# Optimization experiments

Measured on AMD Instinct MI355X. Metric: run time of the kernel, lower is better.

Reference implementation:

```python
import jax, jax.numpy as jnp
import numpy as np

IN_CH = 256
NUM_ANCHORS = 9
NUM_CLASSES = 91
PRIOR_P = 0.01


def conv3x3(x, w, b):
    # x: [N,C,H,W], w: [O,I,3,3], b: [O]
    y = jax.lax.conv_general_dilated(
        x, w, window_strides=(1, 1), padding='SAME',
        dimension_numbers=('NCHW', 'OIHW', 'NCHW'))
    return y + b[None, :, None, None]


def run_head(x, conv_w, conv_b, out_w, out_b, k):
    for i in range(4):
        x = jax.nn.relu(conv3x3(x, conv_w[i], conv_b[i]))
    y = conv3x3(x, out_w, out_b)
    n, _, h, w = y.shape
    # [N, A*k, H, W] -> [N, A, k, H, W] -> [N, H, W, A, k] -> [N, H*W*A, k]
    y = y.reshape(n, -1, k, h, w).transpose(0, 3, 4, 1, 2).reshape(n, -1, k)
    return y


def setup_inputs() -> dict:
    key = jax.random.key(0)
    ks = jax.random.split(key, 16)
    sizes = [128, 64, 32, 16, 8]
    inp = {}
    for i, s in enumerate(sizes):
        inp[f'feat{i}'] = jax.random.normal(ks[i], (2, IN_CH, s, s), dtype=jnp.float32)
    std = 0.01
    inp['cls_conv_w'] = std * jax.random.normal(ks[5], (4, IN_CH, IN_CH, 3, 3), dtype=jnp.float32)
    inp['cls_conv_b'] = jnp.zeros((4, IN_CH), dtype=jnp.float32)
    inp['cls_out_w'] = std * jax.random.normal(ks[6], (NUM_ANCHORS * NUM_CLASSES, IN_CH, 3, 3), dtype=jnp.float32)
    bias_init = -np.log((1.0 - PRIOR_P) / PRIOR_P)
    inp['cls_out_b'] = jnp.full((NUM_ANCHORS * NUM_CLASSES,), bias_init, dtype=jnp.float32)
    inp['reg_conv_w'] = std * jax.random.normal(ks[7], (4, IN_CH, IN_CH, 3, 3), dtype=jnp.float32)
    inp['reg_conv_b'] = jnp.zeros((4, IN_CH), dtype=jnp.float32)
    inp['reg_out_w'] = std * jax.random.normal(ks[8], (NUM_ANCHORS * 4, IN_CH, 3, 3), dtype=jnp.float32)
    inp['reg_out_b'] = jnp.zeros((NUM_ANCHORS * 4,), dtype=jnp.float32)
    return inp


def reference(feat0, feat1, feat2, feat3, feat4,
              cls_conv_w, cls_conv_b, cls_out_w, cls_out_b,
              reg_conv_w, reg_conv_b, reg_out_w, reg_out_b):
    feats = [feat0, feat1, feat2, feat3, feat4]
    cls_logits = jnp.concatenate(
        [run_head(f, cls_conv_w, cls_conv_b, cls_out_w, cls_out_b, NUM_CLASSES) for f in feats],
        axis=1)  # [N, sum(HWA), num_classes]
    bbox_regression = jnp.concatenate(
        [run_head(f, reg_conv_w, reg_conv_b, reg_out_w, reg_out_b, 4) for f in feats],
        axis=1)  # [N, sum(HWA), 4]
    return (cls_logits, bbox_regression)
```

## Files before the change

kernel.cpp:

```cpp
#include <hip/hip_runtime.h>
#include <hip/hip_bf16.h>

typedef __attribute__((ext_vector_type(8))) short   short8;
typedef __attribute__((ext_vector_type(4))) float   floatx4;
typedef __attribute__((ext_vector_type(4))) unsigned short ushort4v;

#define ICH 256


struct Desc {
    int Wd[5];
    int BWd[5];
    int nbXd[5];
    int Moff[5];
    int aoff[5];
    int bstart[6];
};

struct FeatPtrs { const float* f[5]; };


__global__ __launch_bounds__(256)
void convert_feats_all(FeatPtrs fp, Desc d, __hip_bfloat16* __restrict__ out, int n) {
    __shared__ float t[64][65];
    const int p = blockIdx.x * 64;
    int sc = 0;
    while (sc < 4 && p >= d.Moff[sc + 1]) ++sc;
    const int M  = d.Wd[sc] * d.Wd[sc];
    const int p0 = p - d.Moff[sc];
    const float* ib = fp.f[sc] + (size_t)n * ICH * M;
    __hip_bfloat16* ob = out + (size_t)p * ICH;
    const int tid = threadIdx.x;
    const int lo = tid & 63, hi = tid >> 6;
    for (int c0 = 0; c0 < ICH; c0 += 64) {
        #pragma unroll
        for (int r = 0; r < 16; ++r) {
            int ic = hi + 4 * r;
            t[ic][lo] = ib[(size_t)(c0 + ic) * M + p0 + lo];
        }
        __syncthreads();
        #pragma unroll
        for (int r = 0; r < 16; ++r) {
            int pp = hi + 4 * r;
            ob[(size_t)pp * ICH + c0 + lo] = __float2bfloat16(t[lo][pp]);
        }
        __syncthreads();
    }
}

__global__ __launch_bounds__(256)
void convert_wmid(const float* __restrict__ in, __hip_bfloat16* __restrict__ out) {
    int idx = blockIdx.x * 256 + threadIdx.x;
    int ic = idx & 255, r = idx >> 8;
    int oc = r & 255, r2 = r >> 8;
    int s = r2 % 9, l = r2 / 9;
    out[idx] = __float2bfloat16(in[(size_t)((l * 256 + oc) * 256 + ic) * 9 + s]);
}

__global__ __launch_bounds__(256)
void convert_wfin(const float* __restrict__ in, __hip_bfloat16* __restrict__ out,
                  int OC, int OCpad) {
    int idx = blockIdx.x * 256 + threadIdx.x;
    int ic = idx & 255, r = idx >> 8;
    int oc = r % OCpad, s = r / OCpad;
    float v = 0.0f;
    if (oc < OC) v = in[(size_t)(oc * 256 + ic) * 9 + s];
    out[idx] = __float2bfloat16(v);
}

template<bool FINAL>
__global__ __launch_bounds__(256, 2)
void conv_fused(Desc d,
                const __hip_bfloat16* __restrict__ srcC,
                const __hip_bfloat16* __restrict__ srcR,
                const __hip_bfloat16* __restrict__ wC,
                const __hip_bfloat16* __restrict__ wR,
                const float* __restrict__ bC,
                const float* __restrict__ bR,
                __hip_bfloat16* __restrict__ dstC,
                __hip_bfloat16* __restrict__ dstR,
                float* __restrict__ foutC,
                float* __restrict__ foutR,
                int OCLc, int OCLr, int OCc, int OCr, int KOUTc, int KOUTr)
{
    constexpr int HTOT = 180;

    __shared__ short lds_act[HTOT * 64];
    __shared__ short lds_w[128 * 64];

    int bl = blockIdx.x, sc = 0;
    while (bl >= d.bstart[sc + 1]) ++sc;
    const int rb  = bl - d.bstart[sc];
    const int W   = d.Wd[sc], H = W;
    const int BW  = d.BWd[sc], BH = 128 / BW, BWP = BW + 2;
    const int nbX = d.nbXd[sc];
    const int by  = rb / nbX, bx = rb - by * nbX;
    const int y0  = by * BH, x0 = bx * BW;

    int head, oc0;
    if constexpr (FINAL) {
        head = (blockIdx.y == 7) ? 1 : 0;
        oc0  = head ? 0 : blockIdx.y * 128;
    } else {
        head = blockIdx.z;
        oc0  = blockIdx.y * 128;
    }

    const __hip_bfloat16* actin = head ? srcR : srcC;
    const __hip_bfloat16* wsrc  = head ? wR : wC;
    const float*          bias  = head ? bR : bC;
    const int             OCL   = head ? OCLr : OCLc;

    const int tid  = threadIdx.x;
    const int lane = tid & 63, wv = tid >> 6;
    const int mw = wv >> 1, nw = wv & 1;
    const int ln = lane & 15, q = lane >> 4;
    const int sub = tid & 7, grp = tid >> 3;

    const short* actg = (const short*)actin + (size_t)d.Moff[sc] * ICH;
    const short* wg   = (const short*)wsrc;

    int base_a[4], base_b[4];
    #pragma unroll
    for (int j = 0; j < 4; ++j)
        base_a[j] = (mw * 64 + 16 * j + ln) * 64 + q * 8;
    #pragma unroll
    for (int i = 0; i < 4; ++i) {
        int t  = nw * 64 + 16 * i + ln;
        int ty = t / BW, tx = t - ty * BW;
        base_b[i] = ((ty + 1) * BWP + tx + 1) * 64 + q * 8;
    }

    floatx4 acc[4][4] = {};

    short8 wreg[4];
    auto loadw = [&](int s, int icb) {
        #pragma unroll
        for (int it = 0; it < 4; ++it) {
            int ocl = grp + 32 * it;
            wreg[it] = *(const short8*)(wg + ((size_t)(s * OCL + oc0 + ocl) * ICH
                                              + icb * 64 + sub * 8));
        }
    };

    loadw(0, 0);

    for (int icb = 0; icb < 4; ++icb) {
        #pragma unroll
        for (int it = 0; it < 6; ++it) {
            int hp = grp + 32 * it;
            if (hp < HTOT) {
                int hy = hp / BWP, hx = hp - hy * BWP;
                int gy = y0 - 1 + hy, gx = x0 - 1 + hx;
                short8 v = {};
                if ((unsigned)gy < (unsigned)H && (unsigned)gx < (unsigned)W)
                    v = *(const short8*)(actg + ((size_t)(gy * W + gx) * ICH
                                                 + icb * 64 + sub * 8));
                *(short8*)(&lds_act[hp * 64 + sub * 8]) = v;
            }
        }
        #pragma unroll
        for (int s = 0; s < 9; ++s) {
            #pragma unroll
            for (int it = 0; it < 4; ++it)
                *(short8*)(&lds_w[(grp + 32 * it) * 64 + sub * 8]) = wreg[it];
            __syncthreads();
            if (s < 8)          loadw(s + 1, icb);
            else if (icb < 3)   loadw(0, icb + 1);

            const int dy = s / 3 - 1, dx = s % 3 - 1;
            const int soff = (dy * BWP + dx) * 64;
            #pragma unroll
            for (int kk = 0; kk < 2; ++kk) {
                short8 af[4], bf[4];
                #pragma unroll
                for (int j = 0; j < 4; ++j)
                    af[j] = *(const short8*)(&lds_w[base_a[j] + 32 * kk]);
                #pragma unroll
                for (int i = 0; i < 4; ++i)
                    bf[i] = *(const short8*)(&lds_act[base_b[i] + soff + 32 * kk]);
                #pragma unroll
                for (int j = 0; j < 4; ++j)
                    #pragma unroll
                    for (int i = 0; i < 4; ++i)
                        acc[j][i] = __builtin_amdgcn_mfma_f32_16x16x32_bf16(
                            af[j], bf[i], acc[j][i], 0, 0, 0);
            }
            __syncthreads();
        }
    }

    if constexpr (!FINAL) {
        __hip_bfloat16* ob = (head ? dstR : dstC) + (size_t)d.Moff[sc] * ICH;
        #pragma unroll
        for (int j = 0; j < 4; ++j) {
            int oc = oc0 + mw * 64 + 16 * j + q * 4;
            float bv[4];
            #pragma unroll
            for (int r = 0; r < 4; ++r) bv[r] = bias[oc + r];
            #pragma unroll
            for (int i = 0; i < 4; ++i) {
                int t  = nw * 64 + 16 * i + ln;
                int ty = t / BW, tx = t - ty * BW;
                int gy = y0 + ty;
                if (gy < H) {
                    union { ushort4v v; __hip_bfloat16 h[4]; } u;
                    #pragma unroll
                    for (int r = 0; r < 4; ++r)
                        u.h[r] = __float2bfloat16(fmaxf(acc[j][i][r] + bv[r], 0.0f));
                    *(ushort4v*)(ob + (size_t)(gy * W + x0 + tx) * ICH + oc) = u.v;
                }
            }
        }
    } else {
        const int KOUT = head ? KOUTr : KOUTc;
        const int OC   = head ? OCr : OCc;
        float* fb      = head ? foutR : foutC;
        const int aoff = d.aoff[sc];
        #pragma unroll
        for (int j = 0; j < 4; ++j) {
            int ocb = oc0 + mw * 64 + 16 * j + q * 4;
            #pragma unroll
            for (int i = 0; i < 4; ++i) {
                int t  = nw * 64 + 16 * i + ln;
                int ty = t / BW, tx = t - ty * BW;
                int gy = y0 + ty;
                if (gy < H) {
                    int p = gy * W + x0 + tx;
                    #pragma unroll
                    for (int r = 0; r < 4; ++r) {
                        int oc = ocb + r;
                        if (oc < OC) {
                            int a = oc / KOUT, c = oc - a * KOUT;
                            fb[(size_t)(aoff + p * 9 + a) * KOUT + c] =
                                acc[j][i][r] + bias[oc];
                        }
                    }
                }
            }
        }
    }
}


extern "C" void kernel_launch(void* const* d_in, const int* in_sizes, int n_in,
                              void* d_out, int out_size, void* d_ws, size_t ws_size,
                              hipStream_t stream) {
    const float* feats[5];
    for (int i = 0; i < 5; i++) feats[i] = (const float*)d_in[i];
    const float* cls_conv_w = (const float*)d_in[5];
    const float* cls_conv_b = (const float*)d_in[6];
    const float* cls_out_w  = (const float*)d_in[7];
    const float* cls_out_b  = (const float*)d_in[8];
    const float* reg_conv_w = (const float*)d_in[9];
    const float* reg_conv_b = (const float*)d_in[10];
    const float* reg_out_w  = (const float*)d_in[11];
    const float* reg_out_b  = (const float*)d_in[12];

    const int MTOT = 21824;
    const int ATOT = 196416;

    char* wp = (char*)d_ws;
    const size_t ABUF = (size_t)MTOT * ICH * 2;
    __hip_bfloat16* featC = (__hip_bfloat16*)wp; wp += ABUF;
    __hip_bfloat16* actA0 = (__hip_bfloat16*)wp; wp += ABUF;
    __hip_bfloat16* actB0 = (__hip_bfloat16*)wp; wp += ABUF;
    __hip_bfloat16* actA1 = (__hip_bfloat16*)wp; wp += ABUF;
    __hip_bfloat16* wmid0 = (__hip_bfloat16*)wp; wp += (size_t)4 * 9 * 256 * 256 * 2;
    __hip_bfloat16* wmid1 = (__hip_bfloat16*)wp; wp += (size_t)4 * 9 * 256 * 256 * 2;
    __hip_bfloat16* wfc   = (__hip_bfloat16*)wp; wp += (size_t)9 * 896 * 256 * 2;
    __hip_bfloat16* wfr   = (__hip_bfloat16*)wp; wp += (size_t)9 * 128 * 256 * 2;

    convert_wmid<<<4 * 9 * 256, 256, 0, stream>>>(cls_conv_w, wmid0);
    convert_wmid<<<4 * 9 * 256, 256, 0, stream>>>(reg_conv_w, wmid1);
    convert_wfin<<<9 * 896, 256, 0, stream>>>(cls_out_w, wfc, 819, 896);
    convert_wfin<<<9 * 128, 256, 0, stream>>>(reg_out_w, wfr, 36, 128);

    static const Desc d = {
        {128, 64, 32, 16, 8},
        {16, 16, 16, 16, 8},
        {8, 4, 2, 1, 1},
        {0, 16384, 20480, 21504, 21760},
        {0, 147456, 184320, 193536, 195840},
        {0, 128, 160, 168, 170, 171}
    };
    const int NBLK = 171;

    FeatPtrs fp;
    for (int i = 0; i < 5; i++) fp.f[i] = feats[i];

    float* cls_out = (float*)d_out;
    float* reg_out = (float*)d_out + (size_t)2 * ATOT * 91;

    const __hip_bfloat16* srcsC[4] = { featC, actA0, actB0, actA0 };
    __hip_bfloat16*       dstsC[4] = { actA0, actB0, actA0, actB0 };
    const __hip_bfloat16* srcsR[4] = { featC, actA1, featC, actA1 };
    __hip_bfloat16*       dstsR[4] = { actA1, featC, actA1, featC };

    for (int n = 0; n < 2; ++n) {
        convert_feats_all<<<dim3(MTOT / 64), 256, 0, stream>>>(fp, d, featC, n);

        for (int l = 0; l < 4; ++l) {
            conv_fused<false><<<dim3(NBLK, 2, 2), 256, 0, stream>>>(
                d, srcsC[l], srcsR[l],
                wmid0 + (size_t)l * 9 * 256 * 256, wmid1 + (size_t)l * 9 * 256 * 256,
                cls_conv_b + l * 256, reg_conv_b + l * 256,
                dstsC[l], dstsR[l], nullptr, nullptr,
                256, 256, 256, 256, 1, 1);
        }

        conv_fused<true><<<dim3(NBLK, 8, 1), 256, 0, stream>>>(
            d, actB0, featC,
            wfc, wfr, cls_out_b, reg_out_b,
            nullptr, nullptr,
            cls_out + (size_t)n * ATOT * 91, reg_out + (size_t)n * ATOT * 4,
            896, 128, 819, 36, 91, 4);
    }
}
```

Measured before the change: 1.395 ms.

## Swizzle LDS tiles, flatten grid, and raise occupancy target for conv kernel

XOR-swizzles the 16-byte column chunks of both the activation and weight LDS tiles by row index, so MFMA fragment reads hit different banks. Flattens the 3D grid into a 1D grid padded to 176 blocks per channel group, with early exit for padding blocks. Raises the launch-bounds minimum to 4 blocks per CU and replaces the tile divides with shifts. The higher occupancy target may force register spills given the 64 accumulator registers.

```diff
diff --git a/kernel.cpp b/kernel.cpp
--- a/kernel.cpp
+++ b/kernel.cpp
@@ -69,7 +69,7 @@
 }
 
 template<bool FINAL>
-__global__ __launch_bounds__(256, 2)
+__global__ __launch_bounds__(256, 4)
 void conv_fused(Desc d,
                 const __hip_bfloat16* __restrict__ srcC,
                 const __hip_bfloat16* __restrict__ srcR,
@@ -88,23 +88,29 @@
     __shared__ short lds_act[HTOT * 64];
     __shared__ short lds_w[128 * 64];
 
-    int bl = blockIdx.x, sc = 0;
+    const int id = blockIdx.x;
+    const int bl = id % 176;
+    if (bl >= 171) return;
+    const int cg = id / 176;
+
+    int head, oc0;
+    if constexpr (FINAL) {
+        head = (cg == 7) ? 1 : 0;
+        oc0  = head ? 0 : cg * 128;
+    } else {
+        head = cg >> 1;
+        oc0  = (cg & 1) * 128;
+    }
+
+    int sc = 0;
     while (bl >= d.bstart[sc + 1]) ++sc;
     const int rb  = bl - d.bstart[sc];
     const int W   = d.Wd[sc], H = W;
     const int BW  = d.BWd[sc], BH = 128 / BW, BWP = BW + 2;
+    const int bwsh = (BW == 16) ? 4 : 3;
     const int nbX = d.nbXd[sc];
     const int by  = rb / nbX, bx = rb - by * nbX;
     const int y0  = by * BH, x0 = bx * BW;
-
-    int head, oc0;
-    if constexpr (FINAL) {
-        head = (blockIdx.y == 7) ? 1 : 0;
-        oc0  = head ? 0 : blockIdx.y * 128;
-    } else {
-        head = blockIdx.z;
-        oc0  = blockIdx.y * 128;
-    }
 
     const __hip_bfloat16* actin = head ? srcR : srcC;
     const __hip_bfloat16* wsrc  = head ? wR : wC;
@@ -120,15 +126,23 @@
     const short* actg = (const short*)actin + (size_t)d.Moff[sc] * ICH;
     const short* wg   = (const short*)wsrc;
 
-    int base_a[4], base_b[4];
+    const int wsw = (sub ^ (grp & 7)) * 8;
+
+    int rowa[4];
     #pragma unroll
     for (int j = 0; j < 4; ++j)
-        base_a[j] = (mw * 64 + 16 * j + ln) * 64 + q * 8;
+        rowa[j] = (mw * 64 + 16 * j + ln) * 64;
+    int asl[2];
+    #pragma unroll
+    for (int kk = 0; kk < 2; ++kk)
+        asl[kk] = ((q + 4 * kk) ^ (ln & 7)) * 8;
+
+    int prow[4];
     #pragma unroll
     for (int i = 0; i < 4; ++i) {
         int t  = nw * 64 + 16 * i + ln;
-        int ty = t / BW, tx = t - ty * BW;
-        base_b[i] = ((ty + 1) * BWP + tx + 1) * 64 + q * 8;
+        int ty = t >> bwsh, tx = t & (BW - 1);
+        prow[i] = (ty + 1) * BWP + tx + 1;
     }
 
     floatx4 acc[4][4] = {};
@@ -156,29 +170,32 @@
                 if ((unsigned)gy < (unsigned)H && (unsigned)gx < (unsigned)W)
                     v = *(const short8*)(actg + ((size_t)(gy * W + gx) * ICH
                                                  + icb * 64 + sub * 8));
-                *(short8*)(&lds_act[hp * 64 + sub * 8]) = v;
+                *(short8*)(&lds_act[hp * 64 + wsw]) = v;
             }
         }
         #pragma unroll
         for (int s = 0; s < 9; ++s) {
             #pragma unroll
             for (int it = 0; it < 4; ++it)
-                *(short8*)(&lds_w[(grp + 32 * it) * 64 + sub * 8]) = wreg[it];
+                *(short8*)(&lds_w[(grp + 32 * it) * 64 + wsw]) = wreg[it];
             __syncthreads();
             if (s < 8)          loadw(s + 1, icb);
             else if (icb < 3)   loadw(0, icb + 1);
 
             const int dy = s / 3 - 1, dx = s % 3 - 1;
-            const int soff = (dy * BWP + dx) * 64;
+            const int dR = dy * BWP + dx;
             #pragma unroll
             for (int kk = 0; kk < 2; ++kk) {
                 short8 af[4], bf[4];
                 #pragma unroll
                 for (int j = 0; j < 4; ++j)
-                    af[j] = *(const short8*)(&lds_w[base_a[j] + 32 * kk]);
+                    af[j] = *(const short8*)(&lds_w[rowa[j] + asl[kk]]);
                 #pragma unroll
-                for (int i = 0; i < 4; ++i)
-                    bf[i] = *(const short8*)(&lds_act[base_b[i] + soff + 32 * kk]);
+                for (int i = 0; i < 4; ++i) {
+                    int rr = prow[i] + dR;
+                    bf[i] = *(const short8*)(
+                        &lds_act[rr * 64 + (((q + 4 * kk) ^ (rr & 7)) << 3)]);
+                }
                 #pragma unroll
                 for (int j = 0; j < 4; ++j)
                     #pragma unroll
@@ -201,7 +218,7 @@
             #pragma unroll
             for (int i = 0; i < 4; ++i) {
                 int t  = nw * 64 + 16 * i + ln;
-                int ty = t / BW, tx = t - ty * BW;
+                int ty = t >> bwsh, tx = t & (BW - 1);
                 int gy = y0 + ty;
                 if (gy < H) {
                     union { ushort4v v; __hip_bfloat16 h[4]; } u;
@@ -223,7 +240,7 @@
             #pragma unroll
             for (int i = 0; i < 4; ++i) {
                 int t  = nw * 64 + 16 * i + ln;
-                int ty = t / BW, tx = t - ty * BW;
+                int ty = t >> bwsh, tx = t & (BW - 1);
                 int gy = y0 + ty;
                 if (gy < H) {
                     int p = gy * W + x0 + tx;
@@ -284,7 +301,6 @@
         {0, 147456, 184320, 193536, 195840},
         {0, 128, 160, 168, 170, 171}
     };
-    const int NBLK = 171;
 
     FeatPtrs fp;
     for (int i = 0; i < 5; i++) fp.f[i] = feats[i];
@@ -301,7 +317,7 @@
         convert_feats_all<<<dim3(MTOT / 64), 256, 0, stream>>>(fp, d, featC, n);
 
         for (int l = 0; l < 4; ++l) {
-            conv_fused<false><<<dim3(NBLK, 2, 2), 256, 0, stream>>>(
+            conv_fused<false><<<dim3(176 * 4), 256, 0, stream>>>(
                 d, srcsC[l], srcsR[l],
                 wmid0 + (size_t)l * 9 * 256 * 256, wmid1 + (size_t)l * 9 * 256 * 256,
                 cls_conv_b + l * 256, reg_conv_b + l * 256,
@@ -309,7 +325,7 @@
                 256, 256, 256, 256, 1, 1);
         }
 
-        conv_fused<true><<<dim3(NBLK, 8, 1), 256, 0, stream>>>(
+        conv_fused<true><<<dim3(176 * 8), 256, 0, stream>>>(
             d, actB0, featC,
             wfc, wfr, cls_out_b, reg_out_b,
             nullptr, nullptr,
```

Measured after the change: 2.675 ms. +91.7%, slower.
